# Optimization experiments

Measured on AMD Instinct MI355X. Metric: run time of the kernel, lower is better.

The kernel has to match this reference:

```python
import jax, jax.numpy as jnp
import numpy as np

CTX = 2048
N_EMBD = 1024
HEAD = 128

def setup_inputs() -> dict:
    key = jax.random.key(0)
    kx, kq, kk, kv = jax.random.split(key, 4)
    s = 1.0 / np.sqrt(N_EMBD)
    return {
        "x": jax.random.normal(kx, (4, CTX, N_EMBD), dtype=jnp.float32),
        "Wq": jax.random.normal(kq, (N_EMBD, HEAD), dtype=jnp.float32) * s,
        "Wk": jax.random.normal(kk, (N_EMBD, HEAD), dtype=jnp.float32) * s,
        "Wv": jax.random.normal(kv, (N_EMBD, HEAD), dtype=jnp.float32) * s,
    }

def reference(x, Wq, Wk, Wv):
    B, T, C = x.shape
    q = jnp.einsum('btc,ch->bth', x, Wq)
    k = jnp.einsum('btc,ch->bth', x, Wk)
    v = jnp.einsum('btc,ch->bth', x, Wv)
    scale = 1.0 / jnp.sqrt(jnp.asarray(k.shape[-1], dtype=x.dtype))
    wei = jnp.einsum('bth,bsh->bts', q, k) * scale  # [B,T,T]
    causal = jnp.tril(jnp.ones((T, T), dtype=bool))
    wei = jnp.where(causal, wei, jnp.asarray(-jnp.inf, dtype=wei.dtype))
    wei = jax.nn.softmax(wei, axis=-1)
    out = jnp.einsum('bts,bsh->bth', wei, v)
    return out
```

## Files before the change

### kernel.cpp

```cpp
#include <hip/hip_runtime.h>

#define BATCH 4
#define CTX   2048
#define EMB   1024
#define HEAD  128

typedef __attribute__((ext_vector_type(8))) short bf16x8;
typedef __attribute__((ext_vector_type(4))) float f32x4;
typedef const __attribute__((address_space(1))) unsigned int* gas_t;
typedef __attribute__((address_space(3))) unsigned int* las_t;

#define FINF (__builtin_inff())
__device__ inline float fexp2(float x) { return __builtin_amdgcn_exp2f(x); }

__device__ inline void cp16(const void* g, void* l) {
    __builtin_amdgcn_global_load_lds((gas_t)g, (las_t)l, 16, 0, 0);
}

__device__ inline unsigned short f2bf(float f) {
    union { float f; unsigned u; } v; v.f = f;
    unsigned r = v.u + 0x7fffu + ((v.u >> 16) & 1u);
    return (unsigned short)(r >> 16);
}
__device__ inline unsigned pk2(float a, float b) {
    return (unsigned)f2bf(a) | ((unsigned)f2bf(b) << 16);
}
__device__ inline float bf2f(unsigned u16) {
    union { unsigned u; float f; } v; v.u = u16 << 16; return v.f;
}

__global__ __launch_bounds__(256)
void transpose_w_kernel(const float* __restrict__ Wq, const float* __restrict__ Wk,
                        const float* __restrict__ Wv, unsigned short* __restrict__ Wt) {
    const int k0 = blockIdx.x * 64;
    const int h0 = blockIdx.y * 64;
    const int w  = blockIdx.z;
    const float* W = (w == 0) ? Wq : (w == 1) ? Wk : Wv;
    __shared__ float Ts[64][65];
    const int tid = threadIdx.x;
    #pragma unroll
    for (int it = 0; it < 4; ++it) {
        const int kk = (tid >> 4) + it * 16;
        const int c4 = (tid & 15) * 4;
        const float4 f = *(const float4*)&W[(size_t)(k0 + kk) * HEAD + h0 + c4];
        Ts[kk][c4 + 0] = f.x; Ts[kk][c4 + 1] = f.y;
        Ts[kk][c4 + 2] = f.z; Ts[kk][c4 + 3] = f.w;
    }
    __syncthreads();
    const int hr  = tid >> 2;
    const int kc0 = (tid & 3) * 16;
    union { unsigned short s[16]; uint4 q[2]; } tmp;
    #pragma unroll
    for (int i = 0; i < 16; ++i) tmp.s[i] = f2bf(Ts[kc0 + i][hr]);
    unsigned short* dst = &Wt[(size_t)w * HEAD * EMB + (size_t)(h0 + hr) * EMB + k0 + kc0];
    ((uint4*)dst)[0] = tmp.q[0];
    ((uint4*)dst)[1] = tmp.q[1];
}

__global__ __launch_bounds__(64, 1)
void proj_kernel(const float* __restrict__ x, const unsigned short* __restrict__ Wt,
                 unsigned short* __restrict__ qb, unsigned short* __restrict__ kb,
                 unsigned short* __restrict__ vt) {
    __shared__ __align__(16) char smem[24576];
    char* Ab = smem;
    char* Bb = smem + 8192;

    const int wsel = blockIdx.y;
    const int lane = threadIdx.x;
    const int p = lane >> 4, c = lane & 15;
    const int m0 = blockIdx.x * 32;
    const unsigned short* Wp = Wt + (size_t)wsel * HEAD * EMB;

    const int u7  = c & 7;
    const int u2c = (c ^ (c >> 2)) & 3;

    auto stage = [&](int bi, int ks) {
        #pragma unroll
        for (int i = 0; i < 4; ++i) {
            const int f = i * 64 + lane;
            const int r = f >> 3, s = f & 7, q = s ^ (r & 7);
            cp16(&x[(size_t)(m0 + r) * EMB + ks * 32 + q * 4],
                 Ab + bi * 4096 + i * 1024);
        }
        #pragma unroll
        for (int i = 0; i < 8; ++i) {
            const int f = i * 64 + lane;
            const int h = f >> 2, s = f & 3, q = s ^ ((h ^ (h >> 2)) & 3);
            cp16(&Wp[(size_t)h * EMB + ks * 32 + q * 8],
                 Bb + bi * 8192 + i * 1024);
        }
    };
    auto xfrag = [&](const char* Ac, int r) {
        const float4 a0 = *(const float4*)(Ac + r * 128 + (((2 * p)     ^ u7) * 16));
        const float4 a1 = *(const float4*)(Ac + r * 128 + (((2 * p + 1) ^ u7) * 16));
        union { unsigned u[4]; bf16x8 v; } xf;
        xf.u[0] = pk2(a0.x, a0.y); xf.u[1] = pk2(a0.z, a0.w);
        xf.u[2] = pk2(a1.x, a1.y); xf.u[3] = pk2(a1.z, a1.w);
        return xf.v;
    };

    f32x4 acc[2][8];
    #pragma unroll
    for (int i = 0; i < 2; ++i)
        #pragma unroll
        for (int j = 0; j < 8; ++j) acc[i][j] = (f32x4){0.f, 0.f, 0.f, 0.f};

    stage(0, 0);
    for (int ks = 0; ks < 32; ++ks) {
        const int cur = ks & 1;
        __builtin_amdgcn_s_waitcnt(0);
        const char* Ac = Ab + cur * 4096;
        const char* Bc = Bb + cur * 8192;
        bf16x8 xv[2], wf[8];
        #pragma unroll
        for (int mi = 0; mi < 2; ++mi) xv[mi] = xfrag(Ac, mi * 16 + c);
        #pragma unroll
        for (int nt = 0; nt < 8; ++nt)
            wf[nt] = *(const bf16x8*)(Bc + (nt * 16 + c) * 64 + ((p ^ u2c) * 16));
        if (ks + 1 < 32) stage(cur ^ 1, ks + 1);
        if (wsel < 2) {
            #pragma unroll
            for (int mi = 0; mi < 2; ++mi)
                #pragma unroll
                for (int nt = 0; nt < 8; ++nt)
                    acc[mi][nt] = __builtin_amdgcn_mfma_f32_16x16x32_bf16(xv[mi], wf[nt], acc[mi][nt], 0, 0, 0);
        } else {
            #pragma unroll
            for (int n2 = 0; n2 < 2; ++n2)
                #pragma unroll
                for (int mt = 0; mt < 8; ++mt)
                    acc[n2][mt] = __builtin_amdgcn_mfma_f32_16x16x32_bf16(wf[mt], xv[n2], acc[n2][mt], 0, 0, 0);
        }
    }

    if (wsel < 2) {
        unsigned short* outp = (wsel == 0) ? qb : kb;
        #pragma unroll
        for (int mi = 0; mi < 2; ++mi)
            #pragma unroll
            for (int rr = 0; rr < 4; ++rr) {
                unsigned short* orow = outp + (size_t)(m0 + mi * 16 + p * 4 + rr) * HEAD + c;
                #pragma unroll
                for (int nt = 0; nt < 8; ++nt)
                    orow[nt * 16] = f2bf(acc[mi][nt][rr]);
            }
    } else {
        const int bidx = m0 >> 11;
        const int tl   = m0 & (CTX - 1);
        unsigned short* vbp = vt + (size_t)bidx * HEAD * CTX;
        #pragma unroll
        for (int mt = 0; mt < 8; ++mt)
            #pragma unroll
            for (int rr = 0; rr < 4; ++rr) {
                const int h = mt * 16 + p * 4 + rr;
                #pragma unroll
                for (int n2 = 0; n2 < 2; ++n2)
                    vbp[(size_t)h * CTX + tl + n2 * 16 + c] = f2bf(acc[n2][mt][rr]);
            }
    }
}

__global__ __launch_bounds__(256, 2)
void attn_split_kernel(const unsigned short* __restrict__ qb,
                       const unsigned short* __restrict__ kb,
                       const unsigned short* __restrict__ vt,
                       unsigned short* __restrict__ pO,
                       float* __restrict__ pM, float* __restrict__ pL) {
    __shared__ __align__(16) char smem[65536];
    char* Kb = smem;
    char* Vb = smem + 32768;

    const int g = blockIdx.x;
    const int b = blockIdx.y;
    int T, ch;
    if (g < 8)       { T = g;                ch = 0; }
    else if (g < 24) { T = 8  + ((g - 8) >> 1);  ch = (g - 8) & 1; }
    else if (g < 48) { T = 16 + (g - 24) / 3;    ch = (g - 24) % 3; }
    else             { T = 24 + ((g - 48) >> 2); ch = (g - 48) & 3; }
    const int nch    = (T >> 3) + 1;
    const int kstart = ch * 512;
    const int kend   = min(kstart + 512, 64 * (T + 1));
    const int nsteps = (kend - kstart) >> 6;
    const bool lastchunk = (ch == nch - 1);

    const int tid  = threadIdx.x;
    const int wv   = tid >> 6;
    const int lane = tid & 63;
    const int p = lane >> 4, c = lane & 15;
    const int t0 = T * 64;
    const int qg = t0 + wv * 16 + c;
    const int u7 = c & 7;

    const unsigned short* kbat = kb + (size_t)b * CTX * HEAD;
    const unsigned short* vbat = vt + (size_t)b * HEAD * CTX;

    bf16x8 qf[4];
    #pragma unroll
    for (int ks = 0; ks < 4; ++ks)
        qf[ks] = *(const bf16x8*)&qb[((size_t)b * CTX + t0 + wv * 16 + c) * HEAD + ks * 32 + p * 8];

    f32x4 o[8];
    #pragma unroll
    for (int i = 0; i < 8; ++i) o[i] = (f32x4){0.f, 0.f, 0.f, 0.f};
    float m = -FINF, l = 0.f;

    const int  slA = 32 * (p & 1) + c;
    const int  slB = slA + 16;
    const bool thi = (p >> 1) != 0;
    const float scale2 = 0.08838834764831845f * 1.44269504088896340f;

    auto stage = [&](int bi, int js) {
        const unsigned short* kg = kbat + (size_t)(kstart + js * 64) * HEAD;
        #pragma unroll
        for (int i = 0; i < 4; ++i) {
            const int f = i * 256 + tid;
            const int r = f >> 4, s = f & 15, q = s ^ (r & 7);
            cp16(kg + (size_t)r * HEAD + q * 8, Kb + bi * 16384 + (f >> 6) * 1024);
        }
        const unsigned short* vg = vbat + kstart + js * 64;
        #pragma unroll
        for (int i = 0; i < 4; ++i) {
            const int f = i * 256 + tid;
            const int r = f >> 3, s = f & 7, q = s ^ (r & 7);
            cp16(vg + (size_t)r * CTX + q * 8, Vb + bi * 16384 + (f >> 6) * 1024);
        }
    };

    stage(0, 0);
    for (int js = 0; js < nsteps; ++js) {
        const int cur = js & 1;
        __builtin_amdgcn_s_waitcnt(0);
        __syncthreads();

        bf16x8 kfr[4][4];
        #pragma unroll
        for (int nt = 0; nt < 4; ++nt) {
            const char* rp = Kb + cur * 16384 + (nt * 16 + c) * 256;
            #pragma unroll
            for (int ks = 0; ks < 4; ++ks)
                kfr[nt][ks] = *(const bf16x8*)(rp + (((ks * 4 + p) ^ u7) * 16));
        }
        if (js + 1 < nsteps) stage(cur ^ 1, js + 1);

        f32x4 st[4];
        #pragma unroll
        for (int nt = 0; nt < 4; ++nt) st[nt] = (f32x4){0.f, 0.f, 0.f, 0.f};
        #pragma unroll
        for (int ks = 0; ks < 4; ++ks)
            #pragma unroll
            for (int nt = 0; nt < 4; ++nt)
                st[nt] = __builtin_amdgcn_mfma_f32_16x16x32_bf16(kfr[nt][ks], qf[ks], st[nt], 0, 0, 0);

        bf16x8 vfr[2][8];
        #pragma unroll
        for (int mt = 0; mt < 8; ++mt) {
            const char* rp = Vb + cur * 16384 + (mt * 16 + c) * 128;
            #pragma unroll
            for (int ch2 = 0; ch2 < 2; ++ch2)
                vfr[ch2][mt] = *(const bf16x8*)(rp + (((ch2 * 4 + p) ^ u7) * 16));
        }

        float s[4][4];
        float lm = -FINF;
        if (lastchunk && js == nsteps - 1) {
            #pragma unroll
            for (int nt = 0; nt < 4; ++nt)
                #pragma unroll
                for (int r = 0; r < 4; ++r) {
                    const int kv = kstart + js * 64 + nt * 16 + p * 4 + r;
                    float v = st[nt][r] * scale2;
                    v = (kv <= qg) ? v : -FINF;
                    s[nt][r] = v;
                    lm = fmaxf(lm, v);
                }
        } else {
            #pragma unroll
            for (int nt = 0; nt < 4; ++nt)
                #pragma unroll
                for (int r = 0; r < 4; ++r) {
                    const float v = st[nt][r] * scale2;
                    s[nt][r] = v;
                    lm = fmaxf(lm, v);
                }
        }
        lm = fmaxf(lm, __shfl_xor(lm, 16, 64));
        lm = fmaxf(lm, __shfl_xor(lm, 32, 64));
        const float m_new = fmaxf(m, lm);
        const float alpha = fexp2(m - m_new);
        float ls = 0.f;
        #pragma unroll
        for (int nt = 0; nt < 4; ++nt)
            #pragma unroll
            for (int r = 0; r < 4; ++r) {
                const float pv = fexp2(s[nt][r] - m_new);
                s[nt][r] = pv;
                ls += pv;
            }
        ls += __shfl_xor(ls, 16, 64);
        ls += __shfl_xor(ls, 32, 64);
        l = l * alpha + ls;
        m = m_new;
        #pragma unroll
        for (int i = 0; i < 8; ++i) {
            o[i][0] *= alpha; o[i][1] *= alpha;
            o[i][2] *= alpha; o[i][3] *= alpha;
        }
        #pragma unroll
        for (int ch2 = 0; ch2 < 2; ++ch2) {
            const unsigned pa0 = pk2(s[2*ch2][0],     s[2*ch2][1]);
            const unsigned pb0 = pk2(s[2*ch2][2],     s[2*ch2][3]);
            const unsigned pa1 = pk2(s[2*ch2 + 1][0], s[2*ch2 + 1][1]);
            const unsigned pb1 = pk2(s[2*ch2 + 1][2], s[2*ch2 + 1][3]);
            const unsigned u0a = __shfl((int)pa0, slA, 64), u0b = __shfl((int)pa1, slA, 64);
            const unsigned u1a = __shfl((int)pb0, slA, 64), u1b = __shfl((int)pb1, slA, 64);
            const unsigned u2a = __shfl((int)pa0, slB, 64), u2b = __shfl((int)pa1, slB, 64);
            const unsigned u3a = __shfl((int)pb0, slB, 64), u3b = __shfl((int)pb1, slB, 64);
            union { unsigned u[4]; bf16x8 v; } pf;
            pf.u[0] = thi ? u0b : u0a;
            pf.u[1] = thi ? u1b : u1a;
            pf.u[2] = thi ? u2b : u2a;
            pf.u[3] = thi ? u3b : u3a;
            #pragma unroll
            for (int mt = 0; mt < 8; ++mt)
                o[mt] = __builtin_amdgcn_mfma_f32_16x16x32_bf16(vfr[ch2][mt], pf.v, o[mt], 0, 0, 0);
        }
    }

    const size_t pbase = (size_t)(b * 32 + T) * 4 + ch;
    unsigned short* po = pO + pbase * (64 * 128) + (wv * 16 + c) * 128;
    #pragma unroll
    for (int mt = 0; mt < 8; ++mt) {
        union { unsigned short sh[4]; uint2 u; } t;
        #pragma unroll
        for (int r = 0; r < 4; ++r) t.sh[r] = f2bf(o[mt][r]);
        *(uint2*)&po[mt * 16 + p * 4] = t.u;
    }
    if (p == 0) {
        pM[pbase * 64 + wv * 16 + c] = m;
        pL[pbase * 64 + wv * 16 + c] = l;
    }
}

__global__ __launch_bounds__(256)
void attn_merge_kernel(const unsigned short* __restrict__ pO,
                       const float* __restrict__ pM, const float* __restrict__ pL,
                       float* __restrict__ out) {
    const int T = blockIdx.x, b = blockIdx.y;
    const int nch = (T >> 3) + 1;
    const int tid = threadIdx.x;
    const int r   = tid >> 2;
    const int c0  = (tid & 3) * 32;
    const size_t base = (size_t)(b * 32 + T) * 4;

    float mv[4], lv[4];
    float M = -FINF;
    #pragma unroll
    for (int i = 0; i < 4; ++i) {
        if (i < nch) { mv[i] = pM[(base + i) * 64 + r]; lv[i] = pL[(base + i) * 64 + r]; }
        else         { mv[i] = -FINF;                   lv[i] = 0.f; }
        M = fmaxf(M, mv[i]);
    }
    float w[4], L = 0.f;
    #pragma unroll
    for (int i = 0; i < 4; ++i) { w[i] = fexp2(mv[i] - M); L += w[i] * lv[i]; }
    const float inv = 1.f / L;

    float acc[32];
    #pragma unroll
    for (int j = 0; j < 32; ++j) acc[j] = 0.f;
    #pragma unroll
    for (int i = 0; i < 4; ++i) {
        if (i < nch) {
            const unsigned* s32 = (const unsigned*)(pO + (base + i) * (64 * 128) + r * 128 + c0);
            const float wi = w[i];
            #pragma unroll
            for (int jw = 0; jw < 16; ++jw) {
                const unsigned u = s32[jw];
                acc[2 * jw]     += wi * bf2f(u & 0xffffu);
                acc[2 * jw + 1] += wi * bf2f(u >> 16);
            }
        }
    }
    float* orow = out + ((size_t)b * CTX + T * 64 + r) * HEAD + c0;
    #pragma unroll
    for (int j4 = 0; j4 < 8; ++j4) {
        float4 ov = make_float4(acc[4*j4] * inv, acc[4*j4+1] * inv,
                                acc[4*j4+2] * inv, acc[4*j4+3] * inv);
        *(float4*)&orow[4 * j4] = ov;
    }
}

__global__ __launch_bounds__(64, 1)
void attn_kernel(const unsigned short* __restrict__ qb,
                 const unsigned short* __restrict__ kb,
                 const unsigned short* __restrict__ vt,
                 float* __restrict__ out) {
    __shared__ __align__(16) char smem[65536];
    char* Kb = smem;
    char* Vb = smem + 32768;
    const int bx   = blockIdx.x;
    const int b    = bx & 3;
    const int tile = 127 - (bx >> 2);
    const int lane = threadIdx.x;
    const int p = lane >> 4, c = lane & 15;
    const int t0 = tile * 16;
    const int qg = t0 + c;
    const int u7 = c & 7;
    const unsigned short* kbat = kb + (size_t)b * CTX * HEAD;
    const unsigned short* vbat = vt + (size_t)b * HEAD * CTX;
    bf16x8 qf[4];
    #pragma unroll
    for (int ks = 0; ks < 4; ++ks)
        qf[ks] = *(const bf16x8*)&qb[((size_t)b * CTX + t0 + c) * HEAD + ks * 32 + p * 8];
    f32x4 o[8];
    #pragma unroll
    for (int i = 0; i < 8; ++i) o[i] = (f32x4){0.f, 0.f, 0.f, 0.f};
    float m = -FINF, l = 0.f;
    const int  slA = 32 * (p & 1) + c;
    const int  slB = slA + 16;
    const bool thi = (p >> 1) != 0;
    const int  nsteps = (tile + 4) >> 2;
    const float scale2 = 0.08838834764831845f * 1.44269504088896340f;
    auto stage = [&](int bi, int js) {
        const unsigned short* kg = kbat + (size_t)(js * 64) * HEAD;
        #pragma unroll
        for (int i = 0; i < 16; ++i) {
            const int f = i * 64 + lane;
            const int r = f >> 4, s = f & 15, q = s ^ (r & 7);
            cp16(kg + (size_t)r * HEAD + q * 8, Kb + bi * 16384 + i * 1024);
        }
        #pragma unroll
        for (int i = 0; i < 16; ++i) {
            const int f = i * 64 + lane;
            const int r = f >> 3, s = f & 7, q = s ^ (r & 7);
            cp16(vbat + (size_t)r * CTX + js * 64 + q * 8, Vb + bi * 16384 + i * 1024);
        }
    };
    stage(0, 0);
    for (int js = 0; js < nsteps; ++js) {
        const int cur = js & 1;
        __builtin_amdgcn_s_waitcnt(0);
        bf16x8 kfr[4][4], vfr[2][8];
        #pragma unroll
        for (int nt = 0; nt < 4; ++nt) {
            const char* rp = Kb + cur * 16384 + (nt * 16 + c) * 256;
            #pragma unroll
            for (int ks = 0; ks < 4; ++ks)
                kfr[nt][ks] = *(const bf16x8*)(rp + (((ks * 4 + p) ^ u7) * 16));
        }
        #pragma unroll
        for (int mt = 0; mt < 8; ++mt) {
            const char* rp = Vb + cur * 16384 + (mt * 16 + c) * 128;
            #pragma unroll
            for (int ch = 0; ch < 2; ++ch)
                vfr[ch][mt] = *(const bf16x8*)(rp + (((ch * 4 + p) ^ u7) * 16));
        }
        if (js + 1 < nsteps) stage(cur ^ 1, js + 1);
        const int c0 = js * 64;
        f32x4 st[4];
        #pragma unroll
        for (int nt = 0; nt < 4; ++nt) st[nt] = (f32x4){0.f, 0.f, 0.f, 0.f};
        #pragma unroll
        for (int ks = 0; ks < 4; ++ks)
            #pragma unroll
            for (int nt = 0; nt < 4; ++nt)
                st[nt] = __builtin_amdgcn_mfma_f32_16x16x32_bf16(kfr[nt][ks], qf[ks], st[nt], 0, 0, 0);
        float s[4][4];
        float lm = -FINF;
        if (js == nsteps - 1) {
            #pragma unroll
            for (int nt = 0; nt < 4; ++nt)
                #pragma unroll
                for (int r = 0; r < 4; ++r) {
                    const int kv = c0 + nt * 16 + p * 4 + r;
                    float v = st[nt][r] * scale2;
                    v = (kv <= qg) ? v : -FINF;
                    s[nt][r] = v;
                    lm = fmaxf(lm, v);
                }
        } else {
            #pragma unroll
            for (int nt = 0; nt < 4; ++nt)
                #pragma unroll
                for (int r = 0; r < 4; ++r) {
                    const float v = st[nt][r] * scale2;
                    s[nt][r] = v;
                    lm = fmaxf(lm, v);
                }
        }
        lm = fmaxf(lm, __shfl_xor(lm, 16, 64));
        lm = fmaxf(lm, __shfl_xor(lm, 32, 64));
        const float m_new = fmaxf(m, lm);
        const float alpha = fexp2(m - m_new);
        float ls = 0.f;
        #pragma unroll
        for (int nt = 0; nt < 4; ++nt)
            #pragma unroll
            for (int r = 0; r < 4; ++r) {
                const float pv = fexp2(s[nt][r] - m_new);
                s[nt][r] = pv;
                ls += pv;
            }
        ls += __shfl_xor(ls, 16, 64);
        ls += __shfl_xor(ls, 32, 64);
        l = l * alpha + ls;
        m = m_new;
        #pragma unroll
        for (int i = 0; i < 8; ++i) {
            o[i][0] *= alpha; o[i][1] *= alpha;
            o[i][2] *= alpha; o[i][3] *= alpha;
        }
        #pragma unroll
        for (int ch = 0; ch < 2; ++ch) {
            const unsigned pa0 = pk2(s[2*ch][0],     s[2*ch][1]);
            const unsigned pb0 = pk2(s[2*ch][2],     s[2*ch][3]);
            const unsigned pa1 = pk2(s[2*ch + 1][0], s[2*ch + 1][1]);
            const unsigned pb1 = pk2(s[2*ch + 1][2], s[2*ch + 1][3]);
            const unsigned u0a = __shfl((int)pa0, slA, 64), u0b = __shfl((int)pa1, slA, 64);
            const unsigned u1a = __shfl((int)pb0, slA, 64), u1b = __shfl((int)pb1, slA, 64);
            const unsigned u2a = __shfl((int)pa0, slB, 64), u2b = __shfl((int)pa1, slB, 64);
            const unsigned u3a = __shfl((int)pb0, slB, 64), u3b = __shfl((int)pb1, slB, 64);
            union { unsigned u[4]; bf16x8 v; } pf;
            pf.u[0] = thi ? u0b : u0a;
            pf.u[1] = thi ? u1b : u1a;
            pf.u[2] = thi ? u2b : u2a;
            pf.u[3] = thi ? u3b : u3a;
            #pragma unroll
            for (int mt = 0; mt < 8; ++mt)
                o[mt] = __builtin_amdgcn_mfma_f32_16x16x32_bf16(vfr[ch][mt], pf.v, o[mt], 0, 0, 0);
        }
    }
    const float linv = 1.f / l;
    float* orow = out + ((size_t)b * CTX + t0 + c) * HEAD;
    #pragma unroll
    for (int mt = 0; mt < 8; ++mt) {
        float4 ov = make_float4(o[mt][0] * linv, o[mt][1] * linv,
                                o[mt][2] * linv, o[mt][3] * linv);
        *(float4*)&orow[mt * 16 + p * 4] = ov;
    }
}

extern "C" void kernel_launch(void* const* d_in, const int* in_sizes, int n_in,
                              void* d_out, int out_size, void* d_ws, size_t ws_size,
                              hipStream_t stream) {
    const float* x  = (const float*)d_in[0];
    const float* Wq = (const float*)d_in[1];
    const float* Wk = (const float*)d_in[2];
    const float* Wv = (const float*)d_in[3];
    float* out = (float*)d_out;

    unsigned short* Wt = (unsigned short*)d_ws;
    unsigned short* qb = Wt + (size_t)3 * HEAD * EMB;
    unsigned short* kb = qb + (size_t)BATCH * CTX * HEAD;
    unsigned short* vt = kb + (size_t)BATCH * CTX * HEAD;
    unsigned short* pO = vt + (size_t)BATCH * CTX * HEAD;
    float* pM = (float*)(pO + (size_t)BATCH * 32 * 4 * 64 * 128);
    float* pL = pM + (size_t)BATCH * 32 * 4 * 64;

    const size_t need = (size_t)((char*)(pL + BATCH * 32 * 4 * 64) - (char*)d_ws);

    transpose_w_kernel<<<dim3(16, 2, 3), 256, 0, stream>>>(Wq, Wk, Wv, Wt);
    proj_kernel<<<dim3((BATCH * CTX) / 32, 3), 64, 0, stream>>>(x, Wt, qb, kb, vt);
    if (ws_size >= need) {
        attn_split_kernel<<<dim3(80, 4), 256, 0, stream>>>(qb, kb, vt, pO, pM, pL);
        attn_merge_kernel<<<dim3(32, 4), 256, 0, stream>>>(pO, pM, pL, out);
    } else {
        attn_kernel<<<BATCH * (CTX / 16), 64, 0, stream>>>(qb, kb, vt, out);
    }
}
```

Before: 123.1 us.

## Double projection K-step to 64 and compute all projections transposed with vectorized stores

The projection kernel now stages 64-wide K chunks of x and W per iteration instead of 32, which halves the loop trip count and the number of waitcnt barriers. The swizzle patterns are widened to match. All three projections now use the transposed MFMA form (W as A operand), so Q/K outputs can be written as packed 8-byte stores per token instead of scattered 2-byte stores. In exchange LDS use doubles to 48KB per block.

After: 122.7 us. No clear change (-0.3%).

```diff
diff --git a/kernel.cpp b/kernel.cpp
--- a/kernel.cpp
+++ b/kernel.cpp
@@ -61,9 +61,9 @@
 void proj_kernel(const float* __restrict__ x, const unsigned short* __restrict__ Wt,
                  unsigned short* __restrict__ qb, unsigned short* __restrict__ kb,
                  unsigned short* __restrict__ vt) {
-    __shared__ __align__(16) char smem[24576];
+    __shared__ __align__(16) char smem[49152];
     char* Ab = smem;
-    char* Bb = smem + 8192;
+    char* Bb = smem + 16384;
 
     const int wsel = blockIdx.y;
     const int lane = threadIdx.x;
@@ -71,28 +71,29 @@
     const int m0 = blockIdx.x * 32;
     const unsigned short* Wp = Wt + (size_t)wsel * HEAD * EMB;
 
-    const int u7  = c & 7;
-    const int u2c = (c ^ (c >> 2)) & 3;
+    const int uA = c;
+    const int uB = c & 7;
 
     auto stage = [&](int bi, int ks) {
-        #pragma unroll
-        for (int i = 0; i < 4; ++i) {
-            const int f = i * 64 + lane;
-            const int r = f >> 3, s = f & 7, q = s ^ (r & 7);
-            cp16(&x[(size_t)(m0 + r) * EMB + ks * 32 + q * 4],
-                 Ab + bi * 4096 + i * 1024);
-        }
         #pragma unroll
         for (int i = 0; i < 8; ++i) {
             const int f = i * 64 + lane;
-            const int h = f >> 2, s = f & 3, q = s ^ ((h ^ (h >> 2)) & 3);
-            cp16(&Wp[(size_t)h * EMB + ks * 32 + q * 8],
-                 Bb + bi * 8192 + i * 1024);
+            const int r = f >> 4, s = f & 15, q = s ^ (r & 15);
+            cp16(&x[(size_t)(m0 + r) * EMB + ks * 64 + q * 4],
+                 Ab + bi * 8192 + i * 1024);
+        }
+        #pragma unroll
+        for (int i = 0; i < 16; ++i) {
+            const int f = i * 64 + lane;
+            const int h = f >> 3, s = f & 7, q = s ^ (h & 7);
+            cp16(&Wp[(size_t)h * EMB + ks * 64 + q * 8],
+                 Bb + bi * 16384 + i * 1024);
         }
     };
-    auto xfrag = [&](const char* Ac, int r) {
-        const float4 a0 = *(const float4*)(Ac + r * 128 + (((2 * p)     ^ u7) * 16));
-        const float4 a1 = *(const float4*)(Ac + r * 128 + (((2 * p + 1) ^ u7) * 16));
+    auto xfrag = [&](const char* Ac, int r, int kc) {
+        const int g0 = kc * 8 + 2 * p;
+        const float4 a0 = *(const float4*)(Ac + r * 256 + ((g0 ^ uA) * 16));
+        const float4 a1 = *(const float4*)(Ac + r * 256 + (((g0 + 1) ^ uA) * 16));
         union { unsigned u[4]; bf16x8 v; } xf;
         xf.u[0] = pk2(a0.x, a0.y); xf.u[1] = pk2(a0.z, a0.w);
         xf.u[2] = pk2(a1.x, a1.y); xf.u[3] = pk2(a1.z, a1.w);
@@ -106,44 +107,47 @@
         for (int j = 0; j < 8; ++j) acc[i][j] = (f32x4){0.f, 0.f, 0.f, 0.f};
 
     stage(0, 0);
-    for (int ks = 0; ks < 32; ++ks) {
+    for (int ks = 0; ks < 16; ++ks) {
         const int cur = ks & 1;
         __builtin_amdgcn_s_waitcnt(0);
-        const char* Ac = Ab + cur * 4096;
-        const char* Bc = Bb + cur * 8192;
-        bf16x8 xv[2], wf[8];
-        #pragma unroll
-        for (int mi = 0; mi < 2; ++mi) xv[mi] = xfrag(Ac, mi * 16 + c);
-        #pragma unroll
-        for (int nt = 0; nt < 8; ++nt)
-            wf[nt] = *(const bf16x8*)(Bc + (nt * 16 + c) * 64 + ((p ^ u2c) * 16));
-        if (ks + 1 < 32) stage(cur ^ 1, ks + 1);
-        if (wsel < 2) {
-            #pragma unroll
-            for (int mi = 0; mi < 2; ++mi)
-                #pragma unroll
-                for (int nt = 0; nt < 8; ++nt)
-                    acc[mi][nt] = __builtin_amdgcn_mfma_f32_16x16x32_bf16(xv[mi], wf[nt], acc[mi][nt], 0, 0, 0);
-        } else {
-            #pragma unroll
-            for (int n2 = 0; n2 < 2; ++n2)
-                #pragma unroll
-                for (int mt = 0; mt < 8; ++mt)
-                    acc[n2][mt] = __builtin_amdgcn_mfma_f32_16x16x32_bf16(wf[mt], xv[n2], acc[n2][mt], 0, 0, 0);
-        }
+        const char* Ac = Ab + cur * 8192;
+        const char* Bc = Bb + cur * 16384;
+        bf16x8 xv[2][2], wf[8][2];
+        #pragma unroll
+        for (int n2 = 0; n2 < 2; ++n2)
+            #pragma unroll
+            for (int kc = 0; kc < 2; ++kc)
+                xv[n2][kc] = xfrag(Ac, n2 * 16 + c, kc);
+        #pragma unroll
+        for (int nt = 0; nt < 8; ++nt) {
+            const int h = nt * 16 + c;
+            #pragma unroll
+            for (int kc = 0; kc < 2; ++kc)
+                wf[nt][kc] = *(const bf16x8*)(Bc + h * 128 + (((kc * 4 + p) ^ uB) * 16));
+        }
+        if (ks + 1 < 16) stage(cur ^ 1, ks + 1);
+        #pragma unroll
+        for (int kc = 0; kc < 2; ++kc)
+            #pragma unroll
+            for (int mt = 0; mt < 8; ++mt) {
+                acc[0][mt] = __builtin_amdgcn_mfma_f32_16x16x32_bf16(wf[mt][kc], xv[0][kc], acc[0][mt], 0, 0, 0);
+                acc[1][mt] = __builtin_amdgcn_mfma_f32_16x16x32_bf16(wf[mt][kc], xv[1][kc], acc[1][mt], 0, 0, 0);
+            }
     }
 
     if (wsel < 2) {
         unsigned short* outp = (wsel == 0) ? qb : kb;
         #pragma unroll
-        for (int mi = 0; mi < 2; ++mi)
-            #pragma unroll
-            for (int rr = 0; rr < 4; ++rr) {
-                unsigned short* orow = outp + (size_t)(m0 + mi * 16 + p * 4 + rr) * HEAD + c;
+        for (int n2 = 0; n2 < 2; ++n2) {
+            const int token = m0 + n2 * 16 + c;
+            #pragma unroll
+            for (int mt = 0; mt < 8; ++mt) {
+                union { unsigned short sh[4]; uint2 u; } t;
                 #pragma unroll
-                for (int nt = 0; nt < 8; ++nt)
-                    orow[nt * 16] = f2bf(acc[mi][nt][rr]);
+                for (int rr = 0; rr < 4; ++rr) t.sh[rr] = f2bf(acc[n2][mt][rr]);
+                *(uint2*)&outp[(size_t)token * HEAD + mt * 16 + p * 4] = t.u;
             }
+        }
     } else {
         const int bidx = m0 >> 11;
         const int tl   = m0 & (CTX - 1);
```

## Fuse split-KV merge into attention kernel via last-arriving-block atomic counter

Applied to the files above, without the earlier changes.

Removes the separate merge kernel launch. Each split block now publishes its partial output, max and sum, fences, and increments a per-tile atomic counter, and the last-arriving chunk block for a tile performs the softmax merge and writes the final output. This saves one kernel launch and its tail gap, at the cost of a memset of the counters, threadfences, and the merge work running on whichever block finishes last.

After: 193.2 us. +56.9%, slower.

```diff
diff --git a/kernel.cpp b/kernel.cpp
--- a/kernel.cpp
+++ b/kernel.cpp
@@ -165,8 +165,10 @@
                        const unsigned short* __restrict__ kb,
                        const unsigned short* __restrict__ vt,
                        unsigned short* __restrict__ pO,
-                       float* __restrict__ pM, float* __restrict__ pL) {
+                       float* __restrict__ pM, float* __restrict__ pL,
+                       int* __restrict__ pCnt, float* __restrict__ out) {
     __shared__ __align__(16) char smem[65536];
+    __shared__ int sArrive;
     char* Kb = smem;
     char* Vb = smem + 32768;
 
@@ -326,7 +328,8 @@
         }
     }
 
-    const size_t pbase = (size_t)(b * 32 + T) * 4 + ch;
+    const size_t tix   = (size_t)(b * 32 + T);
+    const size_t pbase = tix * 4 + ch;
     unsigned short* po = pO + pbase * (64 * 128) + (wv * 16 + c) * 128;
     #pragma unroll
     for (int mt = 0; mt < 8; ++mt) {
@@ -339,54 +342,54 @@
         pM[pbase * 64 + wv * 16 + c] = m;
         pL[pbase * 64 + wv * 16 + c] = l;
     }
-}
-
-__global__ __launch_bounds__(256)
-void attn_merge_kernel(const unsigned short* __restrict__ pO,
-                       const float* __restrict__ pM, const float* __restrict__ pL,
-                       float* __restrict__ out) {
-    const int T = blockIdx.x, b = blockIdx.y;
-    const int nch = (T >> 3) + 1;
-    const int tid = threadIdx.x;
-    const int r   = tid >> 2;
-    const int c0  = (tid & 3) * 32;
-    const size_t base = (size_t)(b * 32 + T) * 4;
-
-    float mv[4], lv[4];
-    float M = -FINF;
-    #pragma unroll
-    for (int i = 0; i < 4; ++i) {
-        if (i < nch) { mv[i] = pM[(base + i) * 64 + r]; lv[i] = pL[(base + i) * 64 + r]; }
-        else         { mv[i] = -FINF;                   lv[i] = 0.f; }
-        M = fmaxf(M, mv[i]);
-    }
-    float w[4], L = 0.f;
-    #pragma unroll
-    for (int i = 0; i < 4; ++i) { w[i] = fexp2(mv[i] - M); L += w[i] * lv[i]; }
-    const float inv = 1.f / L;
-
-    float acc[32];
-    #pragma unroll
-    for (int j = 0; j < 32; ++j) acc[j] = 0.f;
-    #pragma unroll
-    for (int i = 0; i < 4; ++i) {
-        if (i < nch) {
-            const unsigned* s32 = (const unsigned*)(pO + (base + i) * (64 * 128) + r * 128 + c0);
-            const float wi = w[i];
-            #pragma unroll
-            for (int jw = 0; jw < 16; ++jw) {
-                const unsigned u = s32[jw];
-                acc[2 * jw]     += wi * bf2f(u & 0xffffu);
-                acc[2 * jw + 1] += wi * bf2f(u >> 16);
+
+    __threadfence();
+    __syncthreads();
+    if (tid == 0) sArrive = atomicAdd(&pCnt[tix], 1);
+    __syncthreads();
+    if (sArrive != nch - 1) return;
+    __threadfence();
+
+    {
+        const int r  = tid >> 2;
+        const int c0 = (tid & 3) * 32;
+        const size_t base = tix * 4;
+        float mv[4], lv[4];
+        float M = -FINF;
+        #pragma unroll
+        for (int i = 0; i < 4; ++i) {
+            if (i < nch) { mv[i] = pM[(base + i) * 64 + r]; lv[i] = pL[(base + i) * 64 + r]; }
+            else         { mv[i] = -FINF;                   lv[i] = 0.f; }
+            M = fmaxf(M, mv[i]);
+        }
+        float w[4], L = 0.f;
+        #pragma unroll
+        for (int i = 0; i < 4; ++i) { w[i] = fexp2(mv[i] - M); L += w[i] * lv[i]; }
+        const float inv = 1.f / L;
+
+        float acc[32];
+        #pragma unroll
+        for (int j = 0; j < 32; ++j) acc[j] = 0.f;
+        #pragma unroll
+        for (int i = 0; i < 4; ++i) {
+            if (i < nch) {
+                const unsigned* s32 = (const unsigned*)(pO + (base + i) * (64 * 128) + r * 128 + c0);
+                const float wi = w[i];
+                #pragma unroll
+                for (int jw = 0; jw < 16; ++jw) {
+                    const unsigned u = s32[jw];
+                    acc[2 * jw]     += wi * bf2f(u & 0xffffu);
+                    acc[2 * jw + 1] += wi * bf2f(u >> 16);
+                }
             }
         }
-    }
-    float* orow = out + ((size_t)b * CTX + T * 64 + r) * HEAD + c0;
-    #pragma unroll
-    for (int j4 = 0; j4 < 8; ++j4) {
-        float4 ov = make_float4(acc[4*j4] * inv, acc[4*j4+1] * inv,
-                                acc[4*j4+2] * inv, acc[4*j4+3] * inv);
-        *(float4*)&orow[4 * j4] = ov;
+        float* orow = out + ((size_t)b * CTX + T * 64 + r) * HEAD + c0;
+        #pragma unroll
+        for (int j4 = 0; j4 < 8; ++j4) {
+            float4 ov = make_float4(acc[4*j4] * inv, acc[4*j4+1] * inv,
+                                    acc[4*j4+2] * inv, acc[4*j4+3] * inv);
+            *(float4*)&orow[4 * j4] = ov;
+        }
     }
 }
 
@@ -556,14 +559,15 @@
     unsigned short* pO = vt + (size_t)BATCH * CTX * HEAD;
     float* pM = (float*)(pO + (size_t)BATCH * 32 * 4 * 64 * 128);
     float* pL = pM + (size_t)BATCH * 32 * 4 * 64;
-
-    const size_t need = (size_t)((char*)(pL + BATCH * 32 * 4 * 64) - (char*)d_ws);
+    int*   pCnt = (int*)(pL + (size_t)BATCH * 32 * 4 * 64);
+
+    const size_t need = (size_t)((char*)(pCnt + BATCH * 32) - (char*)d_ws);
 
     transpose_w_kernel<<<dim3(16, 2, 3), 256, 0, stream>>>(Wq, Wk, Wv, Wt);
     proj_kernel<<<dim3((BATCH * CTX) / 32, 3), 64, 0, stream>>>(x, Wt, qb, kb, vt);
     if (ws_size >= need) {
-        attn_split_kernel<<<dim3(80, 4), 256, 0, stream>>>(qb, kb, vt, pO, pM, pL);
-        attn_merge_kernel<<<dim3(32, 4), 256, 0, stream>>>(pO, pM, pL, out);
+        hipMemsetAsync(pCnt, 0, BATCH * 32 * sizeof(int), stream);
+        attn_split_kernel<<<dim3(80, 4), 256, 0, stream>>>(qb, kb, vt, pO, pM, pL, pCnt, out);
     } else {
         attn_kernel<<<BATCH * (CTX / 16), 64, 0, stream>>>(qb, kb, vt, out);
     }
```
